# Performance work log

Measured on AMD Instinct MI355X. Metric: run time of the kernel, lower is better.

The kernel has to match this reference:

```python
import jax, jax.numpy as jnp
import numpy as np

DIM = 1024
DIM_HEAD = 64
HEADS = 16
INNER = DIM_HEAD * HEADS
SCALE = 8.0
EPS_LN = 1e-5
EPS_L2 = 1e-12


def _layernorm(x, gamma):
    mu = jnp.mean(x, axis=-1, keepdims=True)
    var = jnp.var(x, axis=-1, keepdims=True)
    return (x - mu) / jnp.sqrt(var + EPS_LN) * gamma  # beta is a zero buffer


def _l2norm(t):
    n = jnp.linalg.norm(t, axis=-1, keepdims=True)
    return t / jnp.maximum(n, EPS_L2)


def setup_inputs() -> dict:
    key = jax.random.key(0)
    ks = jax.random.split(key, 8)
    b, n = 4, 2048
    x = jax.random.normal(ks[0], (b, n, DIM), dtype=jnp.float32)
    context_mask = jax.random.randint(ks[1], (b, n), 0, 2) > 0
    gamma = jnp.ones((DIM,), dtype=jnp.float32)
    wq = jax.random.normal(ks[2], (DIM, INNER), dtype=jnp.float32) * 0.02
    wkv = jax.random.normal(ks[3], (DIM, 2 * INNER), dtype=jnp.float32) * 0.02
    null_kv = jax.random.normal(ks[4], (2, HEADS, 1, DIM_HEAD), dtype=jnp.float32)
    q_scale = jnp.ones((DIM_HEAD,), dtype=jnp.float32)
    k_scale = jnp.ones((DIM_HEAD,), dtype=jnp.float32)
    wo = jax.random.normal(ks[5], (INNER, DIM), dtype=jnp.float32) * 0.02
    return {"x": x, "context_mask": context_mask, "gamma": gamma, "wq": wq,
            "wkv": wkv, "null_kv": null_kv, "q_scale": q_scale,
            "k_scale": k_scale, "wo": wo}


def reference(x, context_mask, gamma, wq, wkv, null_kv, q_scale, k_scale, wo):
    b, n, _ = x.shape
    xn = _layernorm(x, gamma)
    q = xn @ wq                     # [b, n, inner]
    kv = xn @ wkv                   # self-attention: kv_input = x
    k, v = jnp.split(kv, 2, axis=-1)

    def split_heads(t):
        return t.reshape(b, n, HEADS, DIM_HEAD).transpose(0, 2, 1, 3)  # b h n d

    q, k, v = map(split_heads, (q, k, v))
    nk = jnp.broadcast_to(null_kv[0][None], (b, HEADS, 1, DIM_HEAD))
    nv = jnp.broadcast_to(null_kv[1][None], (b, HEADS, 1, DIM_HEAD))
    k = jnp.concatenate([nk, k], axis=2)  # b h (n+1) d
    v = jnp.concatenate([nv, v], axis=2)

    q = _l2norm(q) * q_scale
    k = _l2norm(k) * k_scale

    sim = jnp.einsum('bhid,bhjd->bhij', q, k) * SCALE  # b h n (n+1)
    mask = jnp.pad(context_mask, ((0, 0), (1, 0)), constant_values=True)  # null kv always visible
    mask_value = -jnp.finfo(sim.dtype).max
    sim = jnp.where(mask[:, None, None, :], sim, mask_value)

    attn = jax.nn.softmax(sim, axis=-1)
    out = jnp.einsum('bhij,bhjd->bhid', attn, v)
    out = out.transpose(0, 2, 1, 3).reshape(b, n, INNER)
    return out @ wo
```

## Files before the change

### kernel.cpp

```cpp
#include <hip/hip_runtime.h>

typedef unsigned short u16;
typedef unsigned int u32;
typedef unsigned long long u64;
typedef __bf16 bf16x8 __attribute__((ext_vector_type(8)));
typedef float f32x4 __attribute__((ext_vector_type(4)));

#define B_ 4
#define N_ 2048
#define D_ 1024
#define H_ 16
#define DH_ 64
#define NKP_ 2112
#define NKT_ 33

__device__ __forceinline__ float bf2f(u16 u) {
  union { u32 i; float f; } v; v.i = ((u32)u) << 16; return v.f;
}
__device__ __forceinline__ u16 f2bf(float f) {
  union { float f; u32 i; } v; v.f = f;
  u32 r = v.i + 0x7fffu + ((v.i >> 16) & 1u);
  return (u16)(r >> 16);
}
__device__ __forceinline__ u32 cvtpk(float a, float b) {
  u32 r;
  asm("v_cvt_pk_bf16_f32 %0, %1, %2" : "=v"(r) : "v"(a), "v"(b));
  return r;
}
__device__ __forceinline__ void load_lds16(const void* g, void* l) {
  __builtin_amdgcn_global_load_lds((const __attribute__((address_space(1))) void*)g,
                                   (__attribute__((address_space(3))) void*)l, 16, 0, 0);
}

__global__ __launch_bounds__(256) void ln_kernel(const float* __restrict__ x,
                                                 const float* __restrict__ gamma,
                                                 u16* __restrict__ xn) {
  int row = blockIdx.x;
  int tid = threadIdx.x, lane = tid & 63, wid = tid >> 6;
  const float4 v = ((const float4*)(x + (size_t)row * D_))[tid];
  float s  = v.x + v.y + v.z + v.w;
  float ss = v.x * v.x + v.y * v.y + v.z * v.z + v.w * v.w;
#pragma unroll
  for (int off = 1; off < 64; off <<= 1) {
    s  += __shfl_xor(s,  off, 64);
    ss += __shfl_xor(ss, off, 64);
  }
  __shared__ float rs[4], rss[4];
  if (lane == 0) { rs[wid] = s; rss[wid] = ss; }
  __syncthreads();
  float S  = rs[0] + rs[1] + rs[2] + rs[3];
  float SS = rss[0] + rss[1] + rss[2] + rss[3];
  float mean = S * (1.0f / D_);
  float var  = SS * (1.0f / D_) - mean * mean;
  float inv  = rsqrtf(var + 1e-5f);
  const float4 g = ((const float4*)gamma)[tid];
  ushort4 o;
  o.x = f2bf((v.x - mean) * inv * g.x);
  o.y = f2bf((v.y - mean) * inv * g.y);
  o.z = f2bf((v.z - mean) * inv * g.z);
  o.w = f2bf((v.w - mean) * inv * g.w);
  *(ushort4*)(xn + (size_t)row * D_ + tid * 4) = o;
}

__global__ __launch_bounds__(256) void wt_kernel(const float* __restrict__ W,
                                                 u16* __restrict__ WT,
                                                 int K, int N) {
  __shared__ float t[32][33];
  int tiles_n = N >> 5;
  int tk = blockIdx.x / tiles_n, tn = blockIdx.x % tiles_n;
  int tx = threadIdx.x & 31, ty = threadIdx.x >> 5;
  int k0 = tk << 5, n0 = tn << 5;
#pragma unroll
  for (int i = 0; i < 4; ++i)
    t[ty + i * 8][tx] = W[(size_t)(k0 + ty + i * 8) * N + n0 + tx];
  __syncthreads();
#pragma unroll
  for (int i = 0; i < 4; ++i)
    WT[(size_t)(n0 + ty + i * 8) * K + k0 + tx] = f2bf(t[tx][ty + i * 8]);
}

__global__ __launch_bounds__(256) void prep_kernel(const int* __restrict__ mask,
                                                   const float* __restrict__ qs,
                                                   const float* __restrict__ ksc,
                                                   const float* __restrict__ null_kv,
                                                   u16* __restrict__ Kb,
                                                   u16* __restrict__ Vt,
                                                   float* __restrict__ cb) {
  __shared__ int cnts[4];
  int bh = blockIdx.x, h = bh & 15;
  int tid = threadIdx.x, lane = tid & 63, wid = tid >> 6;
  if (wid == 0) {
    float kv = null_kv[h * 64 + lane];
    float ss = kv * kv;
#pragma unroll
    for (int off = 1; off < 64; off <<= 1) ss += __shfl_xor(ss, off, 64);
    float inv = 1.0f / fmaxf(sqrtf(ss), 1e-12f);
    Kb[((size_t)bh * NKP_ + 2048) * 64 + lane] = f2bf(kv * inv * ksc[lane]);
    Vt[((size_t)bh * 64 + lane) * NKP_ + 2048] = f2bf(null_kv[1024 + h * 64 + lane]);
  }
  for (int i = tid; i < 63 * 64; i += 256) {
    int r = i >> 6, c = i & 63;
    Kb[((size_t)bh * NKP_ + 2049 + r) * 64 + c] = 0;
  }
  for (int i = tid; i < 64 * 63; i += 256) {
    int d = i / 63, c = i % 63;
    Vt[((size_t)bh * 64 + d) * NKP_ + 2049 + c] = 0;
  }
  if (bh == 0) {
    if (tid < 4) cnts[tid] = 0;
    __syncthreads();
    int c0 = 0, c1 = 0, c2 = 0, c3 = 0;
    for (int i = tid; i < B_ * N_; i += 256) {
      int z = (mask[i] == 0);
      int b = i >> 11;
      if (b == 0) c0 += z; else if (b == 1) c1 += z; else if (b == 2) c2 += z; else c3 += z;
    }
    atomicAdd(&cnts[0], c0); atomicAdd(&cnts[1], c1);
    atomicAdd(&cnts[2], c2); atomicAdd(&cnts[3], c3);
    __syncthreads();
    if (tid == 0) {
      float mw = 0.f;
      for (int i = 0; i < DH_; ++i) mw = fmaxf(mw, fabsf(qs[i] * ksc[i]));
      float cbias = -8.0f * mw * 1.4426950408889634f;
      cb[0] = cbias;
      float e = __builtin_amdgcn_exp2f(cbias);
#pragma unroll
      for (int b = 0; b < 4; ++b) cb[1 + b] = (float)(cnts[b] + 63) * e;
    }
  }
}

__global__ __launch_bounds__(512, 1) void gemm_qkv(const u16* __restrict__ A,
                                                   const u16* __restrict__ Bt,
                                                   u16* __restrict__ Qo,
                                                   u16* __restrict__ Kb,
                                                   u16* __restrict__ Vt,
                                                   const float* __restrict__ qs,
                                                   const float* __restrict__ ksc,
                                                   const int* __restrict__ Mask) {
  __shared__ __attribute__((aligned(16))) u16 dsm[65536];
  int bx = blockIdx.x, by = blockIdx.y;
  int tid = threadIdx.x, lane = tid & 63, wid = tid >> 6;
  int wr = wid >> 2, wc = wid & 3;
  int m0 = bx * 256, n0 = by * 256;
  int wm = wr * 128, wn = wc * 64;
  int la = lane & 15, hi = lane >> 4, crow = hi * 4;
  int sr = lane >> 3;
  int scz = ((lane & 7) ^ (lane >> 3)) * 8;
  f32x4 acc[8][4] = {};

#define QSTAGE(buf, kt)                                                        \
  do {                                                                         \
    int k0_ = (kt) * 64;                                                       \
    u16* ab_ = dsm + (buf) * 32768;                                            \
    _Pragma("unroll")                                                          \
    for (int r4 = 0; r4 < 4; ++r4) {                                           \
      int r_ = r4 * 64 + wid * 8;                   \
      load_lds16(A  + (size_t)(m0 + r_ + sr) * 1024 + k0_ + scz, ab_ + r_ * 64); \
      load_lds16(Bt + (size_t)(n0 + r_ + sr) * 1024 + k0_ + scz, ab_ + 16384 + r_ * 64); \
    }                                                                          \
  } while (0)

  QSTAGE(0, 0);

  for (int kt = 0; kt < 16; ++kt) {
    int buf = kt & 1;
    __builtin_amdgcn_s_barrier();
    if (kt + 1 < 16) {
      QSTAGE(buf ^ 1, kt + 1);
      asm volatile("s_waitcnt vmcnt(8)" ::: "memory");
    } else {
      asm volatile("s_waitcnt vmcnt(0)" ::: "memory");
    }
    __builtin_amdgcn_s_barrier();
    __builtin_amdgcn_sched_barrier(0);
    const u16* a_l = dsm + buf * 32768;
    const u16* b_l = a_l + 16384;
    __builtin_amdgcn_s_setprio(1);
#pragma unroll
    for (int s = 0; s < 2; ++s) {
      int slotbase = s * 4 + hi;
      bf16x8 bfr[4];
#pragma unroll
      for (int nf = 0; nf < 4; ++nf)
        bfr[nf] = *(const bf16x8*)&b_l[(wn + nf * 16 + la) * 64 + ((slotbase ^ (la & 7)) * 8)];
#pragma unroll
      for (int mf = 0; mf < 8; ++mf) {
        bf16x8 af = *(const bf16x8*)&a_l[(wm + mf * 16 + la) * 64 + ((slotbase ^ (la & 7)) * 8)];
#pragma unroll
        for (int nf = 0; nf < 4; ++nf)
          acc[mf][nf] = __builtin_amdgcn_mfma_f32_16x16x32_bf16(af, bfr[nf], acc[mf][nf], 0, 0, 0);
      }
    }
    __builtin_amdgcn_s_setprio(0);
  }
#undef QSTAGE

  int ccol = la;
  if (by < 4) {
    float qsv[4];
#pragma unroll
    for (int nf = 0; nf < 4; ++nf) qsv[nf] = qs[nf * 16 + ccol];
#pragma unroll
    for (int mf = 0; mf < 8; ++mf) {
      float invr[4];
#pragma unroll
      for (int r = 0; r < 4; ++r) {
        float ss = 0.f;
#pragma unroll
        for (int nf = 0; nf < 4; ++nf) ss += acc[mf][nf][r] * acc[mf][nf][r];
#pragma unroll
        for (int off = 1; off < 16; off <<= 1) ss += __shfl_xor(ss, off, 64);
        invr[r] = 1.0f / fmaxf(sqrtf(ss), 1e-12f);
      }
#pragma unroll
      for (int nf = 0; nf < 4; ++nf) {
        int rr = m0 + wm + mf * 16 + crow;
        int cc = by * 256 + wn + nf * 16 + ccol;
#pragma unroll
        for (int r = 0; r < 4; ++r)
          Qo[(size_t)(rr + r) * 1024 + cc] = f2bf(acc[mf][nf][r] * invr[r] * qsv[nf]);
      }
    }
    return;
  }

  int rr0 = m0 + wm;
  int b = rr0 >> 11;
  int seq0 = rr0 & 2047;
  const int* mrow = Mask + b * N_ + seq0;
  if (by < 8) {
    int h = (by - 4) * 4 + wc;
    float kscv[4];
#pragma unroll
    for (int nf = 0; nf < 4; ++nf) kscv[nf] = ksc[nf * 16 + ccol];
    u16* kb = Kb + ((size_t)(b * 16 + h) * NKP_) * 64;
#pragma unroll
    for (int mf = 0; mf < 8; ++mf) {
      float invr[4]; int mvv[4];
#pragma unroll
      for (int r = 0; r < 4; ++r) {
        float ss = 0.f;
#pragma unroll
        for (int nf = 0; nf < 4; ++nf) ss += acc[mf][nf][r] * acc[mf][nf][r];
#pragma unroll
        for (int off = 1; off < 16; off <<= 1) ss += __shfl_xor(ss, off, 64);
        invr[r] = 1.0f / fmaxf(sqrtf(ss), 1e-12f);
        mvv[r] = mrow[mf * 16 + crow + r];
      }
#pragma unroll
      for (int nf = 0; nf < 4; ++nf)
#pragma unroll
        for (int r = 0; r < 4; ++r)
          kb[(size_t)(seq0 + mf * 16 + crow + r) * 64 + nf * 16 + ccol] =
              f2bf(mvv[r] ? acc[mf][nf][r] * invr[r] * kscv[nf] : 0.f);
    }
  } else {
    int h = (by - 8) * 4 + wc;
    __syncthreads();
    u16* tw = dsm + wid * 8192;
#pragma unroll
    for (int mf = 0; mf < 8; ++mf) {
      int mvv[4];
#pragma unroll
      for (int r = 0; r < 4; ++r) mvv[r] = mrow[mf * 16 + crow + r];
#pragma unroll
      for (int nf = 0; nf < 4; ++nf) {
        int d = nf * 16 + ccol;
#pragma unroll
        for (int r = 0; r < 4; ++r) {
          int key = mf * 16 + crow + r;
          tw[d * 128 + ((((key >> 3) ^ (d & 7)) << 3) | (key & 7))] =
              f2bf(mvv[r] ? acc[mf][nf][r] : 0.f);
        }
      }
    }
    u16* vb = Vt + ((size_t)(b * 16 + h) * 64) * NKP_;
    int key0 = seq0;
    int dr = lane >> 3, kc8 = (lane & 7);
#pragma unroll
    for (int j = 0; j < 8; ++j) {
      int d = j * 8 + dr;
#pragma unroll
      for (int half = 0; half < 2; ++half) {
        int kslot = kc8 + half * 8;
        bf16x8 vv = *(const bf16x8*)&tw[d * 128 + (((kslot ^ (d & 7)) & 15) * 8)];
        *(bf16x8*)(vb + (size_t)d * NKP_ + key0 + kslot * 8) = vv;
      }
    }
  }
}

#define GEMM_BODY(A, Bt)                                                       \
  int tid = threadIdx.x, lane = tid & 63, wid = tid >> 6;                      \
  int m0 = blockIdx.x * 128, n0 = blockIdx.y * 128;                            \
  int wm = (wid >> 1) * 64, wn = (wid & 1) * 64;                               \
  int sr = lane >> 3;                                                          \
  int scz = ((lane & 7) ^ (lane >> 3)) * 8;                                    \
  int la = lane & 15, lk = (lane >> 4) * 8;                                    \
  int swz = (la & 7) * 8;                                                      \
  f32x4 acc[4][4] = {};                                                        \
  for (int kt = 0; kt < 16; ++kt) {                                            \
    int k0_ = kt * 64;                                                         \
    __syncthreads();                                                           \
    _Pragma("unroll")                                                          \
    for (int i_ = 0; i_ < 4; ++i_) {                                           \
      int r_ = i_ * 32 + wid * 8;                                              \
      load_lds16(A + (size_t)(m0 + r_ + sr) * 1024 + k0_ + scz, &a_sm[r_ * 64]); \
      load_lds16(Bt + (size_t)(n0 + r_ + sr) * 1024 + k0_ + scz, &b_sm[r_ * 64]); \
    }                                                                          \
    __syncthreads();                                                           \
    _Pragma("unroll")                                                          \
    for (int s = 0; s < 2; ++s) {                                              \
      bf16x8 af[4], bfr[4];                                                    \
      _Pragma("unroll")                                                        \
      for (int mf = 0; mf < 4; ++mf)                                           \
        af[mf] = *(const bf16x8*)&a_sm[(wm + mf * 16 + la) * 64 + ((s * 32 + lk) ^ swz)]; \
      _Pragma("unroll")                                                        \
      for (int nf = 0; nf < 4; ++nf)                                           \
        bfr[nf] = *(const bf16x8*)&b_sm[(wn + nf * 16 + la) * 64 + ((s * 32 + lk) ^ swz)]; \
      _Pragma("unroll")                                                        \
      for (int mf = 0; mf < 4; ++mf)                                           \
        _Pragma("unroll")                                                      \
        for (int nf = 0; nf < 4; ++nf)                                         \
          acc[mf][nf] = __builtin_amdgcn_mfma_f32_16x16x32_bf16(af[mf], bfr[nf], acc[mf][nf], 0, 0, 0); \
    }                                                                          \
  }                                                                            \
  int crow = (lane >> 4) * 4, ccol = lane & 15;

__global__ __launch_bounds__(256) void gemm_out(const u16* __restrict__ A,
                                                const u16* __restrict__ Bt,
                                                float* __restrict__ C) {
  __shared__ __attribute__((aligned(16))) u16 sm[2 * 128 * 64];
  u16* a_sm = sm;
  u16* b_sm = sm + 128 * 64;
  GEMM_BODY(A, Bt)
#pragma unroll
  for (int mf = 0; mf < 4; ++mf)
#pragma unroll
    for (int nf = 0; nf < 4; ++nf) {
      int rr = m0 + wm + mf * 16 + crow;
      int cc = n0 + wn + nf * 16 + ccol;
#pragma unroll
      for (int r = 0; r < 4; ++r) C[(size_t)(rr + r) * 1024 + cc] = acc[mf][nf][r];
    }
}

__global__ __launch_bounds__(512) void attn_kernel(const u16* __restrict__ Q,
                                                   const u16* __restrict__ Kb,
                                                   const u16* __restrict__ Vt,
                                                   const float* __restrict__ cb,
                                                   u16* __restrict__ O) {
  __shared__ __attribute__((aligned(16))) u16 k_sm[2][64 * 64];
  __shared__ __attribute__((aligned(16))) u16 v_sm[2][64 * 64];
  __shared__ __attribute__((aligned(16))) u16 p_sm[8][32 * 64];
  int tid = threadIdx.x, lane = tid & 63, wid = tid >> 6;
  int bh = blockIdx.x, b = bh >> 4, h = bh & 15;
  int q0 = blockIdx.y * 256 + wid * 32;
  int la = lane & 15, lk = (lane >> 4) * 8, crow = (lane >> 4) * 4;
  int swz = (la & 7) * 8;
  int sr = lane >> 3;
  int scz = ((lane & 7) ^ (lane >> 3)) * 8;

  bf16x8 aq[2][2];
#pragma unroll
  for (int qb = 0; qb < 2; ++qb) {
    const u16* qrow = Q + ((size_t)(b * N_) + q0 + qb * 16 + la) * D_ + h * DH_;
#pragma unroll
    for (int s = 0; s < 2; ++s) aq[qb][s] = *(const bf16x8*)(qrow + s * 32 + lk);
  }
  float l[2] = {0.f, 0.f};
  f32x4 o[2][4] = {};
  const u16* Kbh = Kb + (size_t)bh * NKP_ * 64;
  const u16* Vbh = Vt + (size_t)bh * 64 * NKP_;
  const float C1 = 11.541560327111707f;
  const float cbias = cb[0];
  const float lsub = cb[1 + b];

#define STAGE(bb, kt)                                                          \
  do {                                                                         \
    int key0_ = (kt) * 64;                                                     \
    int r_ = wid * 8;                                                          \
    load_lds16(Kbh + (size_t)(key0_ + r_ + sr) * 64 + scz, &k_sm[bb][r_ * 64]); \
    load_lds16(Vbh + (size_t)(r_ + sr) * NKP_ + key0_ + scz, &v_sm[bb][r_ * 64]); \
  } while (0)

  STAGE(0, 0);

#pragma unroll 2
  for (int kt = 0; kt < NKT_; ++kt) {
    int bb = kt & 1;
    __syncthreads();
    if (kt + 1 < NKT_) STAGE(bb ^ 1, kt + 1);

    f32x4 sacc[2][4] = {};
    __builtin_amdgcn_s_setprio(1);
#pragma unroll
    for (int nf = 0; nf < 4; ++nf) {
      bf16x8 bk0 = *(const bf16x8*)&k_sm[bb][(nf * 16 + la) * 64 + (lk ^ swz)];
      bf16x8 bk1 = *(const bf16x8*)&k_sm[bb][(nf * 16 + la) * 64 + ((32 + lk) ^ swz)];
#pragma unroll
      for (int qb = 0; qb < 2; ++qb) {
        sacc[qb][nf] = __builtin_amdgcn_mfma_f32_16x16x32_bf16(bk0, aq[qb][0], sacc[qb][nf], 0, 0, 0);
        sacc[qb][nf] = __builtin_amdgcn_mfma_f32_16x16x32_bf16(bk1, aq[qb][1], sacc[qb][nf], 0, 0, 0);
      }
    }
    __builtin_amdgcn_s_setprio(0);

#pragma unroll
    for (int nf = 0; nf < 4; ++nf) {
      int key = nf * 16 + crow;
#pragma unroll
      for (int qb = 0; qb < 2; ++qb) {
        float p0 = __builtin_amdgcn_exp2f(fmaf(sacc[qb][nf][0], C1, cbias));
        float p1 = __builtin_amdgcn_exp2f(fmaf(sacc[qb][nf][1], C1, cbias));
        float p2 = __builtin_amdgcn_exp2f(fmaf(sacc[qb][nf][2], C1, cbias));
        float p3 = __builtin_amdgcn_exp2f(fmaf(sacc[qb][nf][3], C1, cbias));
        l[qb] += (p0 + p1) + (p2 + p3);
        uint2 pw;
        pw.x = cvtpk(p0, p1);
        pw.y = cvtpk(p2, p3);
        *(uint2*)&p_sm[wid][(qb * 16 + la) * 64 + (key ^ swz)] = pw;
      }
    }

    __builtin_amdgcn_s_setprio(1);
#pragma unroll
    for (int s = 0; s < 2; ++s) {
      bf16x8 bv[4];
#pragma unroll
      for (int dt = 0; dt < 4; ++dt)
        bv[dt] = *(const bf16x8*)&v_sm[bb][(dt * 16 + la) * 64 + ((s * 32 + lk) ^ swz)];
#pragma unroll
      for (int qb = 0; qb < 2; ++qb) {
        bf16x8 ap = *(const bf16x8*)&p_sm[wid][(qb * 16 + la) * 64 + ((s * 32 + lk) ^ swz)];
#pragma unroll
        for (int dt = 0; dt < 4; ++dt)
          o[qb][dt] = __builtin_amdgcn_mfma_f32_16x16x32_bf16(ap, bv[dt], o[qb][dt], 0, 0, 0);
      }
    }
    __builtin_amdgcn_s_setprio(0);
  }
#undef STAGE

#pragma unroll
  for (int qb = 0; qb < 2; ++qb) {
    l[qb] += __shfl_xor(l[qb], 16, 64);
    l[qb] += __shfl_xor(l[qb], 32, 64);
#pragma unroll
    for (int r = 0; r < 4; ++r) {
      float lq = __shfl(l[qb], crow + r, 64) - lsub;
      float inv = 1.0f / lq;
      int n = q0 + qb * 16 + crow + r;
      u16* ob = O + ((size_t)(b * N_) + n) * D_ + h * DH_;
#pragma unroll
      for (int dt = 0; dt < 4; ++dt) ob[dt * 16 + la] = f2bf(o[qb][dt][r] * inv);
    }
  }
}

extern "C" void kernel_launch(void* const* d_in, const int* in_sizes, int n_in,
                              void* d_out, int out_size, void* d_ws, size_t ws_size,
                              hipStream_t stream) {
  (void)in_sizes; (void)n_in; (void)out_size; (void)ws_size;
  const float* x     = (const float*)d_in[0];
  const int*   mask  = (const int*)d_in[1];
  const float* gamma = (const float*)d_in[2];
  const float* wq    = (const float*)d_in[3];
  const float* wkv   = (const float*)d_in[4];
  const float* nkv   = (const float*)d_in[5];
  const float* qs    = (const float*)d_in[6];
  const float* ksc   = (const float*)d_in[7];
  const float* wo    = (const float*)d_in[8];

  char* ws   = (char*)d_ws;
  u16* xn    = (u16*)(ws);
  u16* wqkvT = (u16*)(ws + (16ull << 20));
  u16* wkvT  = wqkvT + 1024 * 1024;
  u16* woT   = (u16*)(ws + (22ull << 20));
  u16* Kb    = (u16*)(ws + (24ull << 20));
  u16* Vt    = (u16*)(ws + (41ull << 20));
  float* cb  = (float*)(ws + (58ull << 20));
  u16* q_tmp = (u16*)d_out;
  u16* attn_out = xn;

  ln_kernel<<<B_ * N_, 256, 0, stream>>>(x, gamma, xn);
  wt_kernel<<<(1024 / 32) * (1024 / 32), 256, 0, stream>>>(wq, wqkvT, 1024, 1024);
  wt_kernel<<<(1024 / 32) * (2048 / 32), 256, 0, stream>>>(wkv, wkvT, 1024, 2048);
  wt_kernel<<<(1024 / 32) * (1024 / 32), 256, 0, stream>>>(wo, woT, 1024, 1024);
  prep_kernel<<<64, 256, 0, stream>>>(mask, qs, ksc, nkv, Kb, Vt, cb);
  gemm_qkv<<<dim3(32, 12), 512, 0, stream>>>(xn, wqkvT, q_tmp, Kb, Vt, qs, ksc, mask);
  attn_kernel<<<dim3(64, 8), 512, 0, stream>>>(q_tmp, Kb, Vt, cb, attn_out);
  gemm_out<<<dim3(64, 8), 256, 0, stream>>>(attn_out, woT, (float*)d_out);
}
```

Before: 207.6 us.

## Deepen QKV GEMM pipeline to four stages with 32-wide K tiles

The QKV projection GEMM now stages K in 32-element tiles across four LDS buffers with three tiles in flight, instead of 64-element tiles double-buffered. The LDS swizzle and fragment indexing are changed to match the 32-column row layout. The aim is to hide global-load latency better, at the cost of twice as many barrier pairs per K sweep and a less even LDS swizzle over four 16-byte slots.

```diff
diff --git a/kernel.cpp b/kernel.cpp
--- a/kernel.cpp
+++ b/kernel.cpp
@@ -144,57 +144,61 @@
   int wr = wid >> 2, wc = wid & 3;
   int m0 = bx * 256, n0 = by * 256;
   int wm = wr * 128, wn = wc * 64;
-  int la = lane & 15, hi = lane >> 4, crow = hi * 4;
-  int sr = lane >> 3;
-  int scz = ((lane & 7) ^ (lane >> 3)) * 8;
+  int la = lane & 15, crow = (lane >> 4) * 4;
+  int rq = lane >> 2;
+  int scz32 = (((lane & 3) ^ ((lane >> 3) & 3))) * 8;
+  int swzoff = (((lane >> 4) ^ ((la >> 1) & 3))) * 8;
   f32x4 acc[8][4] = {};
 
-#define QSTAGE(buf, kt)                                                        \
+#define STAGE32(buf, kt)                                                       \
   do {                                                                         \
-    int k0_ = (kt) * 64;                                                       \
-    u16* ab_ = dsm + (buf) * 32768;                                            \
+    int k0_ = (kt) * 32;                                                       \
+    u16* ab_ = dsm + (buf) * 16384;                                            \
     _Pragma("unroll")                                                          \
-    for (int r4 = 0; r4 < 4; ++r4) {                                           \
-      int r_ = r4 * 64 + wid * 8;                   \
-      load_lds16(A  + (size_t)(m0 + r_ + sr) * 1024 + k0_ + scz, ab_ + r_ * 64); \
-      load_lds16(Bt + (size_t)(n0 + r_ + sr) * 1024 + k0_ + scz, ab_ + 16384 + r_ * 64); \
+    for (int i_ = 0; i_ < 2; ++i_) {                                           \
+      int rb_ = i_ * 128 + wid * 16;                \
+      load_lds16(A  + (size_t)(m0 + rb_ + rq) * 1024 + k0_ + scz32, ab_ + rb_ * 32); \
+      load_lds16(Bt + (size_t)(n0 + rb_ + rq) * 1024 + k0_ + scz32, ab_ + 8192 + rb_ * 32); \
     }                                                                          \
   } while (0)
 
-  QSTAGE(0, 0);
-
-  for (int kt = 0; kt < 16; ++kt) {
-    int buf = kt & 1;
+  STAGE32(0, 0);
+  STAGE32(1, 1);
+  STAGE32(2, 2);
+
+  for (int t = 0; t < 32; ++t) {
+    int buf = t & 3;
     __builtin_amdgcn_s_barrier();
-    if (kt + 1 < 16) {
-      QSTAGE(buf ^ 1, kt + 1);
+    if (t + 3 < 32) {
+      STAGE32((t + 3) & 3, t + 3);
+      asm volatile("s_waitcnt vmcnt(12)" ::: "memory");
+    } else if (t == 29) {
       asm volatile("s_waitcnt vmcnt(8)" ::: "memory");
+    } else if (t == 30) {
+      asm volatile("s_waitcnt vmcnt(4)" ::: "memory");
     } else {
       asm volatile("s_waitcnt vmcnt(0)" ::: "memory");
     }
     __builtin_amdgcn_s_barrier();
     __builtin_amdgcn_sched_barrier(0);
-    const u16* a_l = dsm + buf * 32768;
-    const u16* b_l = a_l + 16384;
+
+    const u16* a_l = dsm + buf * 16384;
+    const u16* b_l = a_l + 8192;
     __builtin_amdgcn_s_setprio(1);
-#pragma unroll
-    for (int s = 0; s < 2; ++s) {
-      int slotbase = s * 4 + hi;
-      bf16x8 bfr[4];
+    bf16x8 bfr[4];
+#pragma unroll
+    for (int nf = 0; nf < 4; ++nf)
+      bfr[nf] = *(const bf16x8*)&b_l[(wn + nf * 16 + la) * 32 + swzoff];
+#pragma unroll
+    for (int mf = 0; mf < 8; ++mf) {
+      bf16x8 af = *(const bf16x8*)&a_l[(wm + mf * 16 + la) * 32 + swzoff];
 #pragma unroll
       for (int nf = 0; nf < 4; ++nf)
-        bfr[nf] = *(const bf16x8*)&b_l[(wn + nf * 16 + la) * 64 + ((slotbase ^ (la & 7)) * 8)];
-#pragma unroll
-      for (int mf = 0; mf < 8; ++mf) {
-        bf16x8 af = *(const bf16x8*)&a_l[(wm + mf * 16 + la) * 64 + ((slotbase ^ (la & 7)) * 8)];
-#pragma unroll
-        for (int nf = 0; nf < 4; ++nf)
-          acc[mf][nf] = __builtin_amdgcn_mfma_f32_16x16x32_bf16(af, bfr[nf], acc[mf][nf], 0, 0, 0);
-      }
+        acc[mf][nf] = __builtin_amdgcn_mfma_f32_16x16x32_bf16(af, bfr[nf], acc[mf][nf], 0, 0, 0);
     }
     __builtin_amdgcn_s_setprio(0);
   }
-#undef QSTAGE
+#undef STAGE32
 
   int ccol = la;
   if (by < 4) {
```

After: 212.1 us. +2.2%, slower.
